# Kernel optimization log

Measured on AMD Instinct MI355X. Metric: run time of the kernel, lower is better.

## Reference

```python
import jax, jax.numpy as jnp
import numpy as np

BLOCK = 4096
V, D = 50304, 1024
EPS = 1e-5


def setup_inputs() -> dict:
    key = jax.random.key(0)
    k1, k2, k3, k4, k5, k6 = jax.random.split(key, 6)
    x = jax.random.randint(k1, (8, 2048), 0, V, dtype=jnp.int64)
    weight_i8 = jax.random.randint(k2, (V, D), 0, 256, dtype=jnp.int32)
    absmax = jax.random.uniform(k3, (V * D // BLOCK,), dtype=jnp.float32)
    code = jax.random.normal(k4, (256,), dtype=jnp.float32)
    ln_weight = jax.random.uniform(k5, (D,), dtype=jnp.float32)
    ln_bias = jax.random.normal(k6, (D,), dtype=jnp.float32)
    return {"x": x, "weight_i8": weight_i8, "absmax": absmax, "code": code,
            "ln_weight": ln_weight, "ln_bias": ln_bias}


def reference(x, weight_i8, absmax, code, ln_weight, ln_bias):
    # Blockwise dequant of the FULL table (faithful to the original forward):
    # each flat block of BLOCK elements shares one absmax scale;
    # int8 codes index a 256-entry code table.
    deq = code[weight_i8.reshape(-1, BLOCK)] * absmax[:, None]   # [nblocks, BLOCK]
    weight_deq = deq.reshape(V, D)
    emb = weight_deq[x]                                           # [B, S, D] gather
    # LayerNorm over the embedding dim with affine params
    mean = jnp.mean(emb, axis=-1, keepdims=True)
    var = jnp.mean(jnp.square(emb - mean), axis=-1, keepdims=True)
    normed = (emb - mean) * jax.lax.rsqrt(var + EPS)
    return normed * ln_weight + ln_bias
```

## Files before the change

### kernel.cpp

```cpp
#include <hip/hip_runtime.h>

#define D 1024
#define EPS 1e-5f

__global__ __launch_bounds__(256) void emb_deq_ln_kernel(
    const int*   __restrict__ x,
    const int*   __restrict__ w,
    const float* __restrict__ absmax,
    const float* __restrict__ code,
    const float* __restrict__ ln_w,
    const float* __restrict__ ln_b,
    float*       __restrict__ out)
{
    __shared__ float code_s[256];
    __shared__ float red[8];
    __shared__ float stats[2];

    const int tid = threadIdx.x;

    code_s[tid] = code[tid];

    const int t = blockIdx.x;
    const int v = x[t];
    const float scale = absmax[v >> 2];

    const int4 wq = ((const int4*)(w + (size_t)v * D))[tid];

    __syncthreads();

    float vals[4];
    vals[0] = code_s[wq.x] * scale;
    vals[1] = code_s[wq.y] * scale;
    vals[2] = code_s[wq.z] * scale;
    vals[3] = code_s[wq.w] * scale;

    float s  = vals[0] + vals[1] + vals[2] + vals[3];
    float ss = vals[0]*vals[0] + vals[1]*vals[1] + vals[2]*vals[2] + vals[3]*vals[3];

    #pragma unroll
    for (int off = 32; off > 0; off >>= 1) {
        s  += __shfl_down(s,  off, 64);
        ss += __shfl_down(ss, off, 64);
    }
    const int lane = tid & 63;
    const int wid  = tid >> 6;
    if (lane == 0) { red[wid * 2] = s; red[wid * 2 + 1] = ss; }
    __syncthreads();

    if (tid == 0) {
        const float ts  = red[0] + red[2] + red[4] + red[6];
        const float tss = red[1] + red[3] + red[5] + red[7];
        const float mean = ts * (1.0f / D);
        const float var  = tss * (1.0f / D) - mean * mean;
        stats[0] = mean;
        stats[1] = rsqrtf(var + EPS);
    }
    __syncthreads();

    const float mean = stats[0];
    const float rstd = stats[1];

    const float4 lw = ((const float4*)ln_w)[tid];
    const float4 lb = ((const float4*)ln_b)[tid];

    float4 o;
    o.x = (vals[0] - mean) * rstd * lw.x + lb.x;
    o.y = (vals[1] - mean) * rstd * lw.y + lb.y;
    o.z = (vals[2] - mean) * rstd * lw.z + lb.z;
    o.w = (vals[3] - mean) * rstd * lw.w + lb.w;

    ((float4*)(out + (size_t)t * D))[tid] = o;
}

extern "C" void kernel_launch(void* const* d_in, const int* in_sizes, int n_in,
                              void* d_out, int out_size, void* d_ws, size_t ws_size,
                              hipStream_t stream) {
    const int*   x      = (const int*)d_in[0];
    const int*   w      = (const int*)d_in[1];
    const float* absmax = (const float*)d_in[2];
    const float* code   = (const float*)d_in[3];
    const float* ln_w   = (const float*)d_in[4];
    const float* ln_b   = (const float*)d_in[5];
    float* out = (float*)d_out;

    const int T = in_sizes[0];

    emb_deq_ln_kernel<<<T, 256, 0, stream>>>(x, w, absmax, code, ln_w, ln_b, out);
}
```

Measured before the change: 278.8 us.

## Process one token per wavefront with grid-stride loop and shuffle-only reduction

Remaps work so each 64-lane wavefront handles a whole token row (16 elements per lane) instead of a 256-thread block per token. This removes the shared-memory reduction and block barriers, and a capped persistent grid loops over tokens so the code table is loaded once per block. The cost is more registers per lane and fewer resident blocks, which could reduce latency hiding.

```diff
diff --git a/kernel.cpp b/kernel.cpp
--- a/kernel.cpp
+++ b/kernel.cpp
@@ -10,66 +10,69 @@
     const float* __restrict__ code,
     const float* __restrict__ ln_w,
     const float* __restrict__ ln_b,
-    float*       __restrict__ out)
+    float*       __restrict__ out,
+    const int    T)
 {
     __shared__ float code_s[256];
-    __shared__ float red[8];
-    __shared__ float stats[2];
-
-    const int tid = threadIdx.x;
-
-    code_s[tid] = code[tid];
-
-    const int t = blockIdx.x;
-    const int v = x[t];
-    const float scale = absmax[v >> 2];
-
-    const int4 wq = ((const int4*)(w + (size_t)v * D))[tid];
-
+    code_s[threadIdx.x] = code[threadIdx.x];
     __syncthreads();
 
-    float vals[4];
-    vals[0] = code_s[wq.x] * scale;
-    vals[1] = code_s[wq.y] * scale;
-    vals[2] = code_s[wq.z] * scale;
-    vals[3] = code_s[wq.w] * scale;
+    const int lane = threadIdx.x & 63;
+    const int wid  = threadIdx.x >> 6;
+    const int wave_global = blockIdx.x * 4 + wid;
+    const int nwave       = gridDim.x * 4;
 
-    float s  = vals[0] + vals[1] + vals[2] + vals[3];
-    float ss = vals[0]*vals[0] + vals[1]*vals[1] + vals[2]*vals[2] + vals[3]*vals[3];
+    for (int t = wave_global; t < T; t += nwave) {
+        const int   v     = x[t];
+        const float scale = absmax[v >> 2];
+        const int4* __restrict__ wr = (const int4*)(w + (size_t)v * D);
 
-    #pragma unroll
-    for (int off = 32; off > 0; off >>= 1) {
-        s  += __shfl_down(s,  off, 64);
-        ss += __shfl_down(ss, off, 64);
+        const int4 q0 = wr[lane];
+        const int4 q1 = wr[64  + lane];
+        const int4 q2 = wr[128 + lane];
+        const int4 q3 = wr[192 + lane];
+
+        float vals[16];
+        vals[0]  = code_s[q0.x]; vals[1]  = code_s[q0.y];
+        vals[2]  = code_s[q0.z]; vals[3]  = code_s[q0.w];
+        vals[4]  = code_s[q1.x]; vals[5]  = code_s[q1.y];
+        vals[6]  = code_s[q1.z]; vals[7]  = code_s[q1.w];
+        vals[8]  = code_s[q2.x]; vals[9]  = code_s[q2.y];
+        vals[10] = code_s[q2.z]; vals[11] = code_s[q2.w];
+        vals[12] = code_s[q3.x]; vals[13] = code_s[q3.y];
+        vals[14] = code_s[q3.z]; vals[15] = code_s[q3.w];
+
+        float s = 0.0f, ss = 0.0f;
+        #pragma unroll
+        for (int i = 0; i < 16; ++i) {
+            const float f = vals[i] * scale;
+            vals[i] = f;
+            s  += f;
+            ss  = fmaf(f, f, ss);
+        }
+
+        #pragma unroll
+        for (int m = 32; m > 0; m >>= 1) {
+            s  += __shfl_xor(s,  m, 64);
+            ss += __shfl_xor(ss, m, 64);
+        }
+
+        const float mean = s * (1.0f / D);
+        const float rstd = rsqrtf(fmaf(-mean, mean, ss * (1.0f / D)) + EPS);
+
+        float* __restrict__ op = out + (size_t)t * D;
+        #pragma unroll
+        for (int k = 0; k < 4; ++k) {
+            const float4 lw = ((const float4*)ln_w)[k * 64 + lane];
+            const float4 lb = ((const float4*)ln_b)[k * 64 + lane];
+            float4 o;
+            o.x = (vals[k * 4 + 0] - mean) * rstd * lw.x + lb.x;
+            o.y = (vals[k * 4 + 1] - mean) * rstd * lw.y + lb.y;
+            o.z = (vals[k * 4 + 2] - mean) * rstd * lw.z + lb.z;
+            o.w = (vals[k * 4 + 3] - mean) * rstd * lw.w + lb.w;
+            ((float4*)op)[k * 64 + lane] = o;
+        }
     }
-    const int lane = tid & 63;
-    const int wid  = tid >> 6;
-    if (lane == 0) { red[wid * 2] = s; red[wid * 2 + 1] = ss; }
-    __syncthreads();
-
-    if (tid == 0) {
-        const float ts  = red[0] + red[2] + red[4] + red[6];
-        const float tss = red[1] + red[3] + red[5] + red[7];
-        const float mean = ts * (1.0f / D);
-        const float var  = tss * (1.0f / D) - mean * mean;
-        stats[0] = mean;
-        stats[1] = rsqrtf(var + EPS);
-    }
-    __syncthreads();
-
-    const float mean = stats[0];
-    const float rstd = stats[1];
-
-    const float4 lw = ((const float4*)ln_w)[tid];
-    const float4 lb = ((const float4*)ln_b)[tid];
-
-    float4 o;
-    o.x = (vals[0] - mean) * rstd * lw.x + lb.x;
-    o.y = (vals[1] - mean) * rstd * lw.y + lb.y;
-    o.z = (vals[2] - mean) * rstd * lw.z + lb.z;
-    o.w = (vals[3] - mean) * rstd * lw.w + lb.w;
-
-    ((float4*)(out + (size_t)t * D))[tid] = o;
 }
 
 extern "C" void kernel_launch(void* const* d_in, const int* in_sizes, int n_in,
@@ -85,5 +88,8 @@
 
     const int T = in_sizes[0];
 
-    emb_deq_ln_kernel<<<T, 256, 0, stream>>>(x, w, absmax, code, ln_w, ln_b, out);
+    int blocks = (T + 3) / 4;
+    if (blocks > 2048) blocks = 2048;
+
+    emb_deq_ln_kernel<<<blocks, 256, 0, stream>>>(x, w, absmax, code, ln_w, ln_b, out, T);
 }
```

Result: no change. 282.4 us (+1.3%).
